# Kernel tuning notes

Measured on AMD Instinct MI355X. Metric: run time of the kernel, lower is better.

Reference implementation:

```python
import jax, jax.numpy as jnp
import numpy as np

N = 100000      # nodes
E = 500000      # edges
NODE_IN = 60
EDGE_IN = 8
H = 256         # hidden
L = 8           # GINEConv layers
G = 64          # graphs in batch
BN_EPS = 1e-5


def setup_inputs() -> dict:
    key = jax.random.key(0)
    ks = jax.random.split(key, 40)
    s = 0.05
    f32 = jnp.float32
    inp = {
        "x": jax.random.normal(ks[0], (N, NODE_IN), f32),
        "edge_index": jax.random.randint(ks[1], (2, E), 0, N),
        "edge_attr": jax.random.normal(ks[2], (E, EDGE_IN), f32),
        "batch": jnp.sort(jax.random.randint(ks[3], (N,), 0, G)),
        # x_proj: Linear(node_in->H) + BatchNorm1d (eval-mode running stats)
        "xproj_W": jax.random.normal(ks[4], (NODE_IN, H), f32) * s,
        "xproj_b": jnp.zeros((H,), f32),
        "xp_gamma": jnp.ones((H,), f32),
        "xp_beta": jnp.zeros((H,), f32),
        "xp_mean": jax.random.normal(ks[5], (H,), f32) * 0.01,
        "xp_var": jax.random.uniform(ks[6], (H,), f32, 0.5, 1.5),
        # stacked GINEConv params (L layers)
        "edge_W": jax.random.normal(ks[7], (L, EDGE_IN, H), f32) * s,
        "edge_b": jnp.zeros((L, H), f32),
        "mlp_W1": jax.random.normal(ks[8], (L, H, H), f32) * s,
        "mlp_b1": jnp.zeros((L, H), f32),
        "mlp_W2": jax.random.normal(ks[9], (L, H, H), f32) * s,
        "mlp_b2": jnp.zeros((L, H), f32),
        "eps": jnp.zeros((L,), f32),  # GINE eps (default 0, not trained)
        # per-layer BatchNorm (eval-mode)
        "bn_gamma": jnp.ones((L, H), f32),
        "bn_beta": jnp.zeros((L, H), f32),
        "bn_mean": jax.random.normal(ks[10], (L, H), f32) * 0.01,
        "bn_var": jax.random.uniform(ks[11], (L, H), f32, 0.5, 1.5),
        # head: Linear(H->H/2) ReLU Dropout Linear(H/2->1)
        "head_W1": jax.random.normal(ks[12], (H, H // 2), f32) * s,
        "head_b1": jnp.zeros((H // 2,), f32),
        "head_W2": jax.random.normal(ks[13], (H // 2, 1), f32) * s,
        "head_b2": jnp.zeros((1,), f32),
    }
    return inp


def _bn(x, gamma, beta, mean, var):
    # eval-mode BatchNorm1d with running stats
    return (x - mean) * (gamma * jax.lax.rsqrt(var + BN_EPS)) + beta


def reference(x, edge_index, edge_attr, batch,
              xproj_W, xproj_b, xp_gamma, xp_beta, xp_mean, xp_var,
              edge_W, edge_b, mlp_W1, mlp_b1, mlp_W2, mlp_b2, eps,
              bn_gamma, bn_beta, bn_mean, bn_var,
              head_W1, head_b1, head_W2, head_b2):
    src, dst = edge_index[0], edge_index[1]  # source -> target aggregation
    # x_proj: Linear + BN + ReLU
    h = jax.nn.relu(_bn(x @ xproj_W + xproj_b, xp_gamma, xp_beta, xp_mean, xp_var))
    for l in range(L):
        # GINEConv: msg = ReLU(x_j + lin(edge_attr)); sum-aggregate at target
        e = edge_attr @ edge_W[l] + edge_b[l]                 # [E,H]
        m = jax.nn.relu(h[src] + e)                           # [E,H] gather + add
        agg = jax.ops.segment_sum(m, dst, num_segments=N)     # [N,H] scatter-add
        z = (1.0 + eps[l]) * h + agg
        z = jax.nn.relu(z @ mlp_W1[l] + mlp_b1[l]) @ mlp_W2[l] + mlp_b2[l]
        # BN + ReLU (dropout is identity in eval)
        h = jax.nn.relu(_bn(z, bn_gamma[l], bn_beta[l], bn_mean[l], bn_var[l]))
    # global_mean_pool over batch ids
    gsum = jax.ops.segment_sum(h, batch, num_segments=G)      # [G,H]
    cnt = jax.ops.segment_sum(jnp.ones((N, 1), h.dtype), batch, num_segments=G)
    g = gsum / jnp.maximum(cnt, 1.0)
    # head MLP -> scalar per graph
    hid = jax.nn.relu(g @ head_W1 + head_b1)
    out = (hid @ head_W2 + head_b2)[:, 0]                     # [G]
    return out
```

## Files before the change

### kernel.cpp

```cpp
#include <hip/hip_runtime.h>

#define N_NODES 100000
#define N_EDGES 500000
#define NODE_IN 60
#define EDGE_IN 8
#define HID 256
#define NLAYERS 8
#define NGRAPH 64
#define BN_EPS 1e-5f
#define SY_PITCH 520

typedef __attribute__((ext_vector_type(4))) float f32x4;
typedef __attribute__((ext_vector_type(4))) short short4v;
typedef __attribute__((ext_vector_type(8))) short short8v;
typedef __attribute__((ext_vector_type(4))) unsigned short u16x4;
typedef unsigned short u16;

__device__ __forceinline__ u16 f2bf(float f) {
    unsigned int u = __builtin_bit_cast(unsigned int, f);
    u += 0x7fffu + ((u >> 16) & 1u);
    return (u16)(u >> 16);
}
__device__ __forceinline__ float bf2f(u16 u) {
    unsigned int x = ((unsigned int)u) << 16;
    return __builtin_bit_cast(float, x);
}
__device__ __forceinline__ float lo_f(unsigned int d) {
    return __builtin_bit_cast(float, d << 16);
}
__device__ __forceinline__ float hi_f(unsigned int d) {
    return __builtin_bit_cast(float, d & 0xffff0000u);
}

__device__ __forceinline__ void g2lds16(const void* g, void* l) {
    __builtin_amdgcn_global_load_lds(
        (const __attribute__((address_space(1))) void*)g,
        (__attribute__((address_space(3))) void*)l, 16, 0, 0);
}

template<int KT, bool WITH_BN>
__global__ __launch_bounds__(256, 2)
void mfma_gemm(const u16* A, const u16* Bt,
               const float* __restrict__ bias,
               const float* __restrict__ gamma, const float* __restrict__ beta,
               const float* __restrict__ mean,  const float* __restrict__ var,
               u16* Cout, int M)
{
    __shared__ u16 smem[24576];
    u16* sA = smem;
    u16* sB = smem + 8192;

    const int tid  = threadIdx.x;
    const int lane = tid & 63;
    const int wv   = tid >> 6;
    const int lrow = lane & 15;
    const int g    = lane >> 4;
    const int m0   = blockIdx.x * 128;
    const int ldab = KT * 128;
    const int lsub = lane >> 3;
    const int gsw  = ((lane & 7) * 16) ^ (lsub << 4);

    f32x4 acc[8][4] = {};

    for (int kt = 0; kt < KT; ++kt) {
        #pragma unroll
        for (int i = 0; i < 4; ++i) {
            const int row = i * 32 + wv * 8 + lsub;
            g2lds16((const char*)A + (size_t)(m0 + row) * ldab + kt * 128 + gsw,
                    (char*)sA + i * 4096 + wv * 1024);
        }
        #pragma unroll
        for (int i = 0; i < 8; ++i) {
            const int row = i * 32 + wv * 8 + lsub;
            g2lds16((const char*)Bt + (size_t)row * ldab + kt * 128 + gsw,
                    (char*)sB + i * 4096 + wv * 1024);
        }
        __syncthreads();

        #pragma unroll
        for (int ks = 0; ks < 2; ++ks) {
            const int off1 = ks * 64 + 8 * g;
            const int off2 = off1 + 32;
            short8v bfrag[4];
            #pragma unroll
            for (int nb = 0; nb < 4; ++nb) {
                const int col = wv * 64 + nb * 16 + lrow;
                const int sw  = (col & 7) << 4;
                short4v lo = *(const short4v*)((const char*)sB + col * 128 + (off1 ^ sw));
                short4v hi = *(const short4v*)((const char*)sB + col * 128 + (off2 ^ sw));
                short8v b;
                b[0] = lo[0]; b[1] = lo[1]; b[2] = lo[2]; b[3] = lo[3];
                b[4] = hi[0]; b[5] = hi[1]; b[6] = hi[2]; b[7] = hi[3];
                bfrag[nb] = b;
            }
            #pragma unroll
            for (int mb = 0; mb < 8; ++mb) {
                const int row = mb * 16 + lrow;
                const int sw  = (row & 7) << 4;
                short4v lo = *(const short4v*)((const char*)sA + row * 128 + (off1 ^ sw));
                short4v hi = *(const short4v*)((const char*)sA + row * 128 + (off2 ^ sw));
                short8v a;
                a[0] = lo[0]; a[1] = lo[1]; a[2] = lo[2]; a[3] = lo[3];
                a[4] = hi[0]; a[5] = hi[1]; a[6] = hi[2]; a[7] = hi[3];
                #pragma unroll
                for (int nb = 0; nb < 4; ++nb)
                    acc[mb][nb] = __builtin_amdgcn_mfma_f32_16x16x32_bf16(a, bfrag[nb], acc[mb][nb], 0, 0, 0);
            }
        }
        __syncthreads();
    }

    #pragma unroll
    for (int mb = 0; mb < 8; ++mb) {
        #pragma unroll
        for (int r = 0; r < 4; ++r) {
            const int row = m0 + mb * 16 + g * 4 + r;
            if (row >= M) continue;
            #pragma unroll
            for (int nb = 0; nb < 4; ++nb) {
                const int col = wv * 64 + nb * 16 + lrow;
                float v = acc[mb][nb][r] + bias[col];
                if constexpr (WITH_BN)
                    v = (v - mean[col]) * (gamma[col] * rsqrtf(var[col] + BN_EPS)) + beta[col];
                v = fmaxf(v, 0.f);
                Cout[(size_t)row * HID + col] = f2bf(v);
            }
        }
    }
}

__global__ __launch_bounds__(256, 2)
void fused_mlp(const u16* __restrict__ Z, const u16* __restrict__ W1t,
               const u16* __restrict__ W2t,
               const float* __restrict__ b1,
               const float* __restrict__ scale2, const float* __restrict__ shift2,
               u16* __restrict__ Hout, int M)
{
    __shared__ u16 smem[37120];
    u16* sA = smem;
    u16* sB = sA + 4096;
    u16* sY = sB + 16384;

    const int tid  = threadIdx.x;
    const int lane = tid & 63;
    const int wv   = tid >> 6;
    const int lrow = lane & 15;
    const int g    = lane >> 4;
    const int m0   = blockIdx.x * 64;
    const int lsub = lane >> 3;
    const int gsw  = ((lane & 7) * 16) ^ (lsub << 4);

    f32x4 acc[4][4] = {};

    for (int kt = 0; kt < 4; ++kt) {
        #pragma unroll
        for (int i = 0; i < 2; ++i) {
            const int row = i * 32 + wv * 8 + lsub;
            g2lds16((const char*)Z + (size_t)(m0 + row) * 512 + kt * 128 + gsw,
                    (char*)sA + i * 4096 + wv * 1024);
        }
        #pragma unroll
        for (int i = 0; i < 8; ++i) {
            const int row = i * 32 + wv * 8 + lsub;
            g2lds16((const char*)W1t + (size_t)row * 512 + kt * 128 + gsw,
                    (char*)sB + i * 4096 + wv * 1024);
        }
        __syncthreads();

        #pragma unroll
        for (int ks = 0; ks < 2; ++ks) {
            const int off1 = ks * 64 + 8 * g;
            const int off2 = off1 + 32;
            short8v bfrag[4];
            #pragma unroll
            for (int nb = 0; nb < 4; ++nb) {
                const int col = wv * 64 + nb * 16 + lrow;
                const int sw  = (col & 7) << 4;
                short4v lo = *(const short4v*)((const char*)sB + col * 128 + (off1 ^ sw));
                short4v hi = *(const short4v*)((const char*)sB + col * 128 + (off2 ^ sw));
                short8v b;
                b[0] = lo[0]; b[1] = lo[1]; b[2] = lo[2]; b[3] = lo[3];
                b[4] = hi[0]; b[5] = hi[1]; b[6] = hi[2]; b[7] = hi[3];
                bfrag[nb] = b;
            }
            #pragma unroll
            for (int mb = 0; mb < 4; ++mb) {
                const int row = mb * 16 + lrow;
                const int sw  = (row & 7) << 4;
                short4v lo = *(const short4v*)((const char*)sA + row * 128 + (off1 ^ sw));
                short4v hi = *(const short4v*)((const char*)sA + row * 128 + (off2 ^ sw));
                short8v a;
                a[0] = lo[0]; a[1] = lo[1]; a[2] = lo[2]; a[3] = lo[3];
                a[4] = hi[0]; a[5] = hi[1]; a[6] = hi[2]; a[7] = hi[3];
                #pragma unroll
                for (int nb = 0; nb < 4; ++nb)
                    acc[mb][nb] = __builtin_amdgcn_mfma_f32_16x16x32_bf16(a, bfrag[nb], acc[mb][nb], 0, 0, 0);
            }
        }
        __syncthreads();
    }

    float b1v[4];
    #pragma unroll
    for (int nb = 0; nb < 4; ++nb) b1v[nb] = b1[wv * 64 + nb * 16 + lrow];
    #pragma unroll
    for (int mb = 0; mb < 4; ++mb) {
        #pragma unroll
        for (int r = 0; r < 4; ++r) {
            const int row = mb * 16 + g * 4 + r;
            #pragma unroll
            for (int nb = 0; nb < 4; ++nb) {
                const int col = wv * 64 + nb * 16 + lrow;
                const float v = fmaxf(acc[mb][nb][r] + b1v[nb], 0.f);
                *(u16*)((char*)sY + row * SY_PITCH + col * 2) = f2bf(v);
            }
        }
    }
    __syncthreads();

    f32x4 acc2[4][4] = {};
    for (int kt2 = 0; kt2 < 4; ++kt2) {
        #pragma unroll
        for (int i = 0; i < 8; ++i) {
            const int row = i * 32 + wv * 8 + lsub;
            g2lds16((const char*)W2t + (size_t)row * 512 + kt2 * 128 + gsw,
                    (char*)sB + i * 4096 + wv * 1024);
        }
        __syncthreads();

        #pragma unroll
        for (int ks = 0; ks < 2; ++ks) {
            const int off1 = ks * 64 + 8 * g;
            const int off2 = off1 + 32;
            const int yo1  = kt2 * 128 + off1;
            const int yo2  = yo1 + 32;
            short8v bfrag[4];
            #pragma unroll
            for (int nb = 0; nb < 4; ++nb) {
                const int col = wv * 64 + nb * 16 + lrow;
                const int sw  = (col & 7) << 4;
                short4v lo = *(const short4v*)((const char*)sB + col * 128 + (off1 ^ sw));
                short4v hi = *(const short4v*)((const char*)sB + col * 128 + (off2 ^ sw));
                short8v b;
                b[0] = lo[0]; b[1] = lo[1]; b[2] = lo[2]; b[3] = lo[3];
                b[4] = hi[0]; b[5] = hi[1]; b[6] = hi[2]; b[7] = hi[3];
                bfrag[nb] = b;
            }
            #pragma unroll
            for (int mb = 0; mb < 4; ++mb) {
                const int row = mb * 16 + lrow;
                short4v lo = *(const short4v*)((const char*)sY + row * SY_PITCH + yo1);
                short4v hi = *(const short4v*)((const char*)sY + row * SY_PITCH + yo2);
                short8v a;
                a[0] = lo[0]; a[1] = lo[1]; a[2] = lo[2]; a[3] = lo[3];
                a[4] = hi[0]; a[5] = hi[1]; a[6] = hi[2]; a[7] = hi[3];
                #pragma unroll
                for (int nb = 0; nb < 4; ++nb)
                    acc2[mb][nb] = __builtin_amdgcn_mfma_f32_16x16x32_bf16(a, bfrag[nb], acc2[mb][nb], 0, 0, 0);
            }
        }
        __syncthreads();
    }

    float scl[4], shf[4];
    #pragma unroll
    for (int nb = 0; nb < 4; ++nb) {
        const int col = wv * 64 + nb * 16 + lrow;
        scl[nb] = scale2[col];
        shf[nb] = shift2[col];
    }
    #pragma unroll
    for (int mb = 0; mb < 4; ++mb) {
        #pragma unroll
        for (int r = 0; r < 4; ++r) {
            const int row = m0 + mb * 16 + g * 4 + r;
            if (row >= M) continue;
            #pragma unroll
            for (int nb = 0; nb < 4; ++nb) {
                const int col = wv * 64 + nb * 16 + lrow;
                const float v = fmaxf(acc2[mb][nb][r] * scl[nb] + shf[nb], 0.f);
                Hout[(size_t)row * HID + col] = f2bf(v);
            }
        }
    }
}

__global__ __launch_bounds__(256)
void convw_kernel(const float* __restrict__ W, u16* __restrict__ Wt)
{
    size_t i = (size_t)blockIdx.x * 256 + threadIdx.x;
    const int mat = (int)(i >> 16);
    const int idx = (int)(i & 65535);
    const int n = idx >> 8, k = idx & 255;
    Wt[i] = f2bf(W[(size_t)mat * 65536 + (size_t)k * 256 + n]);
}

__global__ __launch_bounds__(256)
void convwx_kernel(const float* __restrict__ W, u16* __restrict__ Wt)
{
    int i = blockIdx.x * 256 + threadIdx.x;
    const int n = i >> 6, k = i & 63;
    Wt[i] = (k < NODE_IN) ? f2bf(W[(size_t)k * HID + n]) : (u16)0;
}

__global__ __launch_bounds__(256)
void convx_kernel(const float* __restrict__ x, u16* __restrict__ xbf)
{
    size_t i = (size_t)blockIdx.x * 256 + threadIdx.x;
    if (i >= (size_t)N_NODES * 64) return;
    const int n = (int)(i >> 6), k = (int)(i & 63);
    xbf[i] = (k < NODE_IN) ? f2bf(x[(size_t)n * NODE_IN + k]) : (u16)0;
}

__global__ __launch_bounds__(256)
void bnfold_kernel(const float* __restrict__ b2, const float* __restrict__ gamma,
                   const float* __restrict__ beta, const float* __restrict__ mean,
                   const float* __restrict__ var,
                   float* __restrict__ scale, float* __restrict__ shift)
{
    int i = blockIdx.x * 256 + threadIdx.x;
    if (i >= NLAYERS * HID) return;
    const float s = gamma[i] * rsqrtf(var[i] + BN_EPS);
    scale[i] = s;
    shift[i] = (b2[i] - mean[i]) * s + beta[i];
}

__global__ __launch_bounds__(256)
void deg_count_kernel(const int* __restrict__ dst, int* __restrict__ deg, int E)
{
    int e = blockIdx.x * 256 + threadIdx.x;
    if (e < E) atomicAdd(&deg[dst[e]], 1);
}

__global__ __launch_bounds__(256)
void scan1_kernel(const int* __restrict__ deg, int* __restrict__ rowptr,
                  int* __restrict__ bsum, int n)
{
    __shared__ int s[256];
    const int tid = threadIdx.x;
    const int i = blockIdx.x * 256 + tid;
    const int v = (i < n) ? deg[i] : 0;
    s[tid] = v;
    __syncthreads();
    #pragma unroll
    for (int d = 1; d < 256; d <<= 1) {
        int t = (tid >= d) ? s[tid - d] : 0;
        __syncthreads();
        s[tid] += t;
        __syncthreads();
    }
    if (i < n) rowptr[i] = s[tid] - v;
    if (tid == 255) bsum[blockIdx.x] = s[255];
}

__global__ void scan2_kernel(int* bsum, int nb, int* rowptr, int n)
{
    if (threadIdx.x == 0 && blockIdx.x == 0) {
        int run = 0;
        for (int j = 0; j < nb; ++j) { int t = bsum[j]; bsum[j] = run; run += t; }
        rowptr[n] = run;
    }
}

__global__ __launch_bounds__(256)
void scan3_kernel(int* __restrict__ rowptr, const int* __restrict__ bsum, int n)
{
    int i = blockIdx.x * 256 + threadIdx.x;
    if (i < n) rowptr[i] += bsum[i >> 8];
}

__global__ __launch_bounds__(256)
void scatter_kernel(const int* __restrict__ src, const int* __restrict__ dst,
                    const float* __restrict__ ea,
                    const int* __restrict__ rowptr, int* __restrict__ fill,
                    int* __restrict__ esrc, u16* __restrict__ eap, int E)
{
    int e = blockIdx.x * 256 + threadIdx.x;
    if (e >= E) return;
    const int d = dst[e];
    const int pos = rowptr[d] + atomicAdd(&fill[d], 1);
    esrc[pos] = src[e];
    const float4 a0 = *(const float4*)&ea[(size_t)e * EDGE_IN];
    const float4 a1 = *(const float4*)&ea[(size_t)e * EDGE_IN + 4];
    u16x4 p0, p1;
    p0[0] = f2bf(a0.x); p0[1] = f2bf(a0.y); p0[2] = f2bf(a0.z); p0[3] = f2bf(a0.w);
    p1[0] = f2bf(a1.x); p1[1] = f2bf(a1.y); p1[2] = f2bf(a1.z); p1[3] = f2bf(a1.w);
    *(u16x4*)&eap[(size_t)pos * EDGE_IN]     = p0;
    *(u16x4*)&eap[(size_t)pos * EDGE_IN + 4] = p1;
}

__global__ __launch_bounds__(256, 8)
void agg_kernel(const u16* __restrict__ h, const u16* __restrict__ eap,
                const int* __restrict__ rowptr, const int* __restrict__ esrc,
                const float* __restrict__ W, const float* __restrict__ b,
                const float* __restrict__ eps, int l, u16* __restrict__ z)
{
    const int lane  = threadIdx.x & 63;
    const int wv    = threadIdx.x >> 6;
    const int c0    = lane * 4;
    const int lofsB = lane * 8;

    f32x4 Wr[EDGE_IN];
    #pragma unroll
    for (int k = 0; k < EDGE_IN; ++k) Wr[k] = *(const f32x4*)&W[k * HID + c0];
    const f32x4 br = *(const f32x4*)&b[c0];
    const float e1 = 1.0f + eps[l];

    for (int n = blockIdx.x * 4 + wv; n < N_NODES; n += gridDim.x * 4) {
        const int beg = __builtin_amdgcn_readfirstlane(rowptr[n]);
        const int end = __builtin_amdgcn_readfirstlane(rowptr[n + 1]);
        const int end1 = end - 1;

        const u16x4 hv = *(const u16x4*)&h[(size_t)n * HID + c0];
        float a0 = e1 * bf2f(hv[0]), a1 = e1 * bf2f(hv[1]);
        float a2 = e1 * bf2f(hv[2]), a3 = e1 * bf2f(hv[3]);

        for (int i0 = beg; i0 < end; i0 += 4) {
            int idx0 = i0;
            int idx1 = (i0 + 1 < end) ? i0 + 1 : end1;
            int idx2 = (i0 + 2 < end) ? i0 + 2 : end1;
            int idx3 = (i0 + 3 < end) ? i0 + 3 : end1;

            const int sb0 = __builtin_amdgcn_readfirstlane(esrc[idx0]) << 9;
            const int sb1 = __builtin_amdgcn_readfirstlane(esrc[idx1]) << 9;
            const int sb2 = __builtin_amdgcn_readfirstlane(esrc[idx2]) << 9;
            const int sb3 = __builtin_amdgcn_readfirstlane(esrc[idx3]) << 9;

            u16x4 hs0 = *(const u16x4*)((const char*)h + (unsigned)(sb0 + lofsB));
            u16x4 hs1 = *(const u16x4*)((const char*)h + (unsigned)(sb1 + lofsB));
            u16x4 hs2 = *(const u16x4*)((const char*)h + (unsigned)(sb2 + lofsB));
            u16x4 hs3 = *(const u16x4*)((const char*)h + (unsigned)(sb3 + lofsB));

            uint4 t0 = *(const uint4*)&eap[(size_t)idx0 * EDGE_IN];
            uint4 t1 = *(const uint4*)&eap[(size_t)idx1 * EDGE_IN];
            uint4 t2 = *(const uint4*)&eap[(size_t)idx2 * EDGE_IN];
            uint4 t3 = *(const uint4*)&eap[(size_t)idx3 * EDGE_IN];

            #pragma unroll
            for (int j = 0; j < 4; ++j) {
                if (i0 + j < end) {
                    const uint4 tt = (j == 0) ? t0 : (j == 1) ? t1 : (j == 2) ? t2 : t3;
                    const u16x4 hh = (j == 0) ? hs0 : (j == 1) ? hs1 : (j == 2) ? hs2 : hs3;
                    const unsigned dx = __builtin_amdgcn_readfirstlane((int)tt.x);
                    const unsigned dy = __builtin_amdgcn_readfirstlane((int)tt.y);
                    const unsigned dz = __builtin_amdgcn_readfirstlane((int)tt.z);
                    const unsigned dw = __builtin_amdgcn_readfirstlane((int)tt.w);
                    f32x4 ev = br;
                    ev += lo_f(dx) * Wr[0];
                    ev += hi_f(dx) * Wr[1];
                    ev += lo_f(dy) * Wr[2];
                    ev += hi_f(dy) * Wr[3];
                    ev += lo_f(dz) * Wr[4];
                    ev += hi_f(dz) * Wr[5];
                    ev += lo_f(dw) * Wr[6];
                    ev += hi_f(dw) * Wr[7];
                    a0 += fmaxf(bf2f(hh[0]) + ev[0], 0.f);
                    a1 += fmaxf(bf2f(hh[1]) + ev[1], 0.f);
                    a2 += fmaxf(bf2f(hh[2]) + ev[2], 0.f);
                    a3 += fmaxf(bf2f(hh[3]) + ev[3], 0.f);
                }
            }
        }
        u16x4 o;
        o[0] = f2bf(a0); o[1] = f2bf(a1); o[2] = f2bf(a2); o[3] = f2bf(a3);
        *(u16x4*)&z[(size_t)n * HID + c0] = o;
    }
}

__global__ __launch_bounds__(256)
void pool_kernel(const u16* __restrict__ h, const int* __restrict__ batch,
                 float* __restrict__ gsum, int* __restrict__ cnt, int n)
{
    const int lane = threadIdx.x & 63;
    const int wv   = threadIdx.x >> 6;
    const int c0   = lane * 4;
    const int n0   = blockIdx.x * 64;

    f32x4 acc = {0.f, 0.f, 0.f, 0.f};
    int gcur = -1;
    int c = 0;

    for (int i = wv; i < 64; i += 4) {
        const int node = n0 + i;
        if (node >= n) break;
        const int g = __builtin_amdgcn_readfirstlane(batch[node]);
        if (g != gcur) {
            if (gcur >= 0) {
                atomicAdd(&gsum[gcur * HID + c0 + 0], acc[0]);
                atomicAdd(&gsum[gcur * HID + c0 + 1], acc[1]);
                atomicAdd(&gsum[gcur * HID + c0 + 2], acc[2]);
                atomicAdd(&gsum[gcur * HID + c0 + 3], acc[3]);
                if (lane == 0) atomicAdd(&cnt[gcur], c);
            }
            acc = (f32x4){0.f, 0.f, 0.f, 0.f};
            c = 0;
            gcur = g;
        }
        const u16x4 hv = *(const u16x4*)&h[(size_t)node * HID + c0];
        acc[0] += bf2f(hv[0]);
        acc[1] += bf2f(hv[1]);
        acc[2] += bf2f(hv[2]);
        acc[3] += bf2f(hv[3]);
        c++;
    }
    if (gcur >= 0) {
        atomicAdd(&gsum[gcur * HID + c0 + 0], acc[0]);
        atomicAdd(&gsum[gcur * HID + c0 + 1], acc[1]);
        atomicAdd(&gsum[gcur * HID + c0 + 2], acc[2]);
        atomicAdd(&gsum[gcur * HID + c0 + 3], acc[3]);
        if (lane == 0) atomicAdd(&cnt[gcur], c);
    }
}

__global__ __launch_bounds__(128)
void head_kernel(const float* __restrict__ gsum, const int* __restrict__ cnt,
                 const float* __restrict__ W1, const float* __restrict__ b1,
                 const float* __restrict__ W2, const float* __restrict__ b2,
                 float* __restrict__ out)
{
    const int gi = blockIdx.x;
    const int j = threadIdx.x;
    __shared__ float gs[HID];
    __shared__ float red[128];

    const float c = fmaxf((float)cnt[gi], 1.0f);
    gs[j]       = gsum[gi * HID + j] / c;
    gs[j + 128] = gsum[gi * HID + 128 + j] / c;
    __syncthreads();

    float acc = b1[j];
    #pragma unroll 8
    for (int k = 0; k < HID; ++k) acc += gs[k] * W1[k * 128 + j];
    acc = fmaxf(acc, 0.f);
    red[j] = acc * W2[j];
    __syncthreads();
    for (int s = 64; s > 0; s >>= 1) {
        if (j < s) red[j] += red[j + s];
        __syncthreads();
    }
    if (j == 0) out[gi] = red[0] + b2[0];
}

extern "C" void kernel_launch(void* const* d_in, const int* in_sizes, int n_in,
                              void* d_out, int out_size, void* d_ws, size_t ws_size,
                              hipStream_t stream)
{
    const float* x         = (const float*)d_in[0];
    const int*   ei        = (const int*)d_in[1];
    const float* edge_attr = (const float*)d_in[2];
    const int*   batch     = (const int*)d_in[3];
    const float* xproj_W   = (const float*)d_in[4];
    const float* xproj_b   = (const float*)d_in[5];
    const float* xp_gamma  = (const float*)d_in[6];
    const float* xp_beta   = (const float*)d_in[7];
    const float* xp_mean   = (const float*)d_in[8];
    const float* xp_var    = (const float*)d_in[9];
    const float* edge_W    = (const float*)d_in[10];
    const float* edge_b    = (const float*)d_in[11];
    const float* mlp_W1    = (const float*)d_in[12];
    const float* mlp_b1    = (const float*)d_in[13];
    const float* mlp_W2    = (const float*)d_in[14];
    const float* mlp_b2    = (const float*)d_in[15];
    const float* eps       = (const float*)d_in[16];
    const float* bn_gamma  = (const float*)d_in[17];
    const float* bn_beta   = (const float*)d_in[18];
    const float* bn_mean   = (const float*)d_in[19];
    const float* bn_var    = (const float*)d_in[20];
    const float* head_W1   = (const float*)d_in[21];
    const float* head_b1   = (const float*)d_in[22];
    const float* head_W2   = (const float*)d_in[23];
    const float* head_b2   = (const float*)d_in[24];
    float* out = (float*)d_out;

    const int* srcI = ei;
    const int* dstI = ei + N_EDGES;

    char* w = (char*)d_ws;
    u16*   h      = (u16*)w;                 w += (size_t)N_NODES * HID * 2;
    u16*   zy     = (u16*)w;                 w += (size_t)N_NODES * HID * 2;
    u16*   xbf    = (u16*)w;                 w += (size_t)N_NODES * 64 * 2;
    u16*   Wt1    = (u16*)w;                 w += (size_t)NLAYERS * 65536 * 2;
    u16*   Wt2    = (u16*)w;                 w += (size_t)NLAYERS * 65536 * 2;
    u16*   Wxt    = (u16*)w;                 w += 16384 * 2;
    float* scale2 = (float*)w;               w += NLAYERS * HID * 4;
    float* shift2 = (float*)w;               w += NLAYERS * HID * 4;
    int*   rowptr = (int*)w;                 w += 100032 * 4;
    int*   deg    = (int*)w;                 w += 100032 * 4;
    int*   fill   = (int*)w;                 w += 100032 * 4;
    int*   bsum   = (int*)w;                 w += 512 * 4;
    int*   esrc   = (int*)w;                 w += (size_t)N_EDGES * 4;
    u16*   eap    = (u16*)w;                 w += (size_t)N_EDGES * EDGE_IN * 2;
    float* gsum   = (float*)w;               w += NGRAPH * HID * 4;
    int*   cnt    = (int*)w;                 w += NGRAPH * 4;

    convw_kernel<<<2048, 256, 0, stream>>>(mlp_W1, Wt1);
    convw_kernel<<<2048, 256, 0, stream>>>(mlp_W2, Wt2);
    convwx_kernel<<<64, 256, 0, stream>>>(xproj_W, Wxt);
    convx_kernel<<<25000, 256, 0, stream>>>(x, xbf);
    bnfold_kernel<<<8, 256, 0, stream>>>(mlp_b2, bn_gamma, bn_beta, bn_mean, bn_var,
                                         scale2, shift2);

    hipMemsetAsync(deg, 0, 2 * 100032 * sizeof(int), stream);
    deg_count_kernel<<<(N_EDGES + 255) / 256, 256, 0, stream>>>(dstI, deg, N_EDGES);
    scan1_kernel<<<391, 256, 0, stream>>>(deg, rowptr, bsum, N_NODES);
    scan2_kernel<<<1, 64, 0, stream>>>(bsum, 391, rowptr, N_NODES);
    scan3_kernel<<<391, 256, 0, stream>>>(rowptr, bsum, N_NODES);
    scatter_kernel<<<(N_EDGES + 255) / 256, 256, 0, stream>>>(
        srcI, dstI, edge_attr, rowptr, fill, esrc, eap, N_EDGES);

    mfma_gemm<1, true><<<(N_NODES + 127) / 128, 256, 0, stream>>>(
        xbf, Wxt, xproj_b, xp_gamma, xp_beta, xp_mean, xp_var, h, N_NODES);

    const int fgrid = (N_NODES + 63) / 64;
    for (int l = 0; l < NLAYERS; ++l) {
        agg_kernel<<<2048, 256, 0, stream>>>(
            h, eap, rowptr, esrc,
            edge_W + (size_t)l * EDGE_IN * HID, edge_b + (size_t)l * HID,
            eps, l, zy);
        fused_mlp<<<fgrid, 256, 0, stream>>>(
            zy, Wt1 + (size_t)l * 65536, Wt2 + (size_t)l * 65536,
            mlp_b1 + (size_t)l * HID, scale2 + (size_t)l * HID, shift2 + (size_t)l * HID,
            h, N_NODES);
    }

    hipMemsetAsync(gsum, 0, (NGRAPH * HID + NGRAPH) * sizeof(float), stream);
    pool_kernel<<<(N_NODES + 63) / 64, 256, 0, stream>>>(h, batch, gsum, cnt, N_NODES);
    head_kernel<<<NGRAPH, 128, 0, stream>>>(gsum, cnt, head_W1, head_b1, head_W2, head_b2, out);
}
```

Baseline: 1.126 ms.

## Prepack MLP weights in MFMA fragment order and read them directly from global

Weights are repacked at setup into per-lane MFMA B-fragment order, so the fused MLP kernel loads B fragments straight from global memory (cached in L2/L1) instead of staging the full 256x256 weight tiles through LDS every k-step. The whole 64-row Z tile is loaded once up front, and shared memory is cut to about 33KB with sZ and sY aliased, which removes per-k-step barriers. Occupancy is raised to 3 blocks per SM. The trade-off is that every block now does redundant global/L1 reads of the weights and depends on cache hit rates, and the higher occupancy target may cause register pressure.

Measured after the change: 1.064 ms, median of 3. 1.06x faster.

```diff
diff --git a/kernel.cpp b/kernel.cpp
--- a/kernel.cpp
+++ b/kernel.cpp
@@ -129,17 +129,16 @@
     }
 }
 
-__global__ __launch_bounds__(256, 2)
-void fused_mlp(const u16* __restrict__ Z, const u16* __restrict__ W1t,
-               const u16* __restrict__ W2t,
+__global__ __launch_bounds__(256, 3)
+void fused_mlp(const u16* __restrict__ Z, const u16* __restrict__ W1p,
+               const u16* __restrict__ W2p,
                const float* __restrict__ b1,
                const float* __restrict__ scale2, const float* __restrict__ shift2,
                u16* __restrict__ Hout, int M)
 {
-    __shared__ u16 smem[37120];
-    u16* sA = smem;
-    u16* sB = sA + 4096;
-    u16* sY = sB + 16384;
+    __shared__ u16 smem[16640];
+    u16* sZ = smem;
+    u16* sY = smem;
 
     const int tid  = threadIdx.x;
     const int lane = tid & 63;
@@ -150,23 +149,20 @@
     const int lsub = lane >> 3;
     const int gsw  = ((lane & 7) * 16) ^ (lsub << 4);
 
-    f32x4 acc[4][4] = {};
-
+    #pragma unroll
     for (int kt = 0; kt < 4; ++kt) {
         #pragma unroll
         for (int i = 0; i < 2; ++i) {
             const int row = i * 32 + wv * 8 + lsub;
             g2lds16((const char*)Z + (size_t)(m0 + row) * 512 + kt * 128 + gsw,
-                    (char*)sA + i * 4096 + wv * 1024);
-        }
-        #pragma unroll
-        for (int i = 0; i < 8; ++i) {
-            const int row = i * 32 + wv * 8 + lsub;
-            g2lds16((const char*)W1t + (size_t)row * 512 + kt * 128 + gsw,
-                    (char*)sB + i * 4096 + wv * 1024);
-        }
-        __syncthreads();
-
+                    (char*)sZ + kt * 8192 + i * 4096 + wv * 1024);
+        }
+    }
+    __syncthreads();
+
+    f32x4 acc[4][4] = {};
+    #pragma unroll
+    for (int kt = 0; kt < 4; ++kt) {
         #pragma unroll
         for (int ks = 0; ks < 2; ++ks) {
             const int off1 = ks * 64 + 8 * g;
@@ -174,21 +170,20 @@
             short8v bfrag[4];
             #pragma unroll
             for (int nb = 0; nb < 4; ++nb) {
-                const int col = wv * 64 + nb * 16 + lrow;
-                const int sw  = (col & 7) << 4;
-                short4v lo = *(const short4v*)((const char*)sB + col * 128 + (off1 ^ sw));
-                short4v hi = *(const short4v*)((const char*)sB + col * 128 + (off2 ^ sw));
+                const int cb = wv * 4 + nb;
+                u16x4 lo = *(const u16x4*)&W1p[((((kt * 2 + ks) * 2 + 0) * 16 + cb) << 8) + lane * 4];
+                u16x4 hi = *(const u16x4*)&W1p[((((kt * 2 + ks) * 2 + 1) * 16 + cb) << 8) + lane * 4];
                 short8v b;
-                b[0] = lo[0]; b[1] = lo[1]; b[2] = lo[2]; b[3] = lo[3];
-                b[4] = hi[0]; b[5] = hi[1]; b[6] = hi[2]; b[7] = hi[3];
+                b[0] = (short)lo[0]; b[1] = (short)lo[1]; b[2] = (short)lo[2]; b[3] = (short)lo[3];
+                b[4] = (short)hi[0]; b[5] = (short)hi[1]; b[6] = (short)hi[2]; b[7] = (short)hi[3];
                 bfrag[nb] = b;
             }
             #pragma unroll
             for (int mb = 0; mb < 4; ++mb) {
                 const int row = mb * 16 + lrow;
                 const int sw  = (row & 7) << 4;
-                short4v lo = *(const short4v*)((const char*)sA + row * 128 + (off1 ^ sw));
-                short4v hi = *(const short4v*)((const char*)sA + row * 128 + (off2 ^ sw));
+                short4v lo = *(const short4v*)((const char*)sZ + kt * 8192 + row * 128 + (off1 ^ sw));
+                short4v hi = *(const short4v*)((const char*)sZ + kt * 8192 + row * 128 + (off2 ^ sw));
                 short8v a;
                 a[0] = lo[0]; a[1] = lo[1]; a[2] = lo[2]; a[3] = lo[3];
                 a[4] = hi[0]; a[5] = hi[1]; a[6] = hi[2]; a[7] = hi[3];
@@ -197,8 +192,8 @@
                     acc[mb][nb] = __builtin_amdgcn_mfma_f32_16x16x32_bf16(a, bfrag[nb], acc[mb][nb], 0, 0, 0);
             }
         }
-        __syncthreads();
-    }
+    }
+    __syncthreads();
 
     float b1v[4];
     #pragma unroll
@@ -219,31 +214,22 @@
     __syncthreads();
 
     f32x4 acc2[4][4] = {};
+    #pragma unroll
     for (int kt2 = 0; kt2 < 4; ++kt2) {
-        #pragma unroll
-        for (int i = 0; i < 8; ++i) {
-            const int row = i * 32 + wv * 8 + lsub;
-            g2lds16((const char*)W2t + (size_t)row * 512 + kt2 * 128 + gsw,
-                    (char*)sB + i * 4096 + wv * 1024);
-        }
-        __syncthreads();
-
         #pragma unroll
         for (int ks = 0; ks < 2; ++ks) {
             const int off1 = ks * 64 + 8 * g;
-            const int off2 = off1 + 32;
             const int yo1  = kt2 * 128 + off1;
             const int yo2  = yo1 + 32;
             short8v bfrag[4];
             #pragma unroll
             for (int nb = 0; nb < 4; ++nb) {
-                const int col = wv * 64 + nb * 16 + lrow;
-                const int sw  = (col & 7) << 4;
-                short4v lo = *(const short4v*)((const char*)sB + col * 128 + (off1 ^ sw));
-                short4v hi = *(const short4v*)((const char*)sB + col * 128 + (off2 ^ sw));
+                const int cb = wv * 4 + nb;
+                u16x4 lo = *(const u16x4*)&W2p[((((kt2 * 2 + ks) * 2 + 0) * 16 + cb) << 8) + lane * 4];
+                u16x4 hi = *(const u16x4*)&W2p[((((kt2 * 2 + ks) * 2 + 1) * 16 + cb) << 8) + lane * 4];
                 short8v b;
-                b[0] = lo[0]; b[1] = lo[1]; b[2] = lo[2]; b[3] = lo[3];
-                b[4] = hi[0]; b[5] = hi[1]; b[6] = hi[2]; b[7] = hi[3];
+                b[0] = (short)lo[0]; b[1] = (short)lo[1]; b[2] = (short)lo[2]; b[3] = (short)lo[3];
+                b[4] = (short)hi[0]; b[5] = (short)hi[1]; b[6] = (short)hi[2]; b[7] = (short)hi[3];
                 bfrag[nb] = b;
             }
             #pragma unroll
@@ -259,7 +245,6 @@
                     acc2[mb][nb] = __builtin_amdgcn_mfma_f32_16x16x32_bf16(a, bfrag[nb], acc2[mb][nb], 0, 0, 0);
             }
         }
-        __syncthreads();
     }
 
     float scl[4], shf[4];
@@ -286,13 +271,20 @@
 }
 
 __global__ __launch_bounds__(256)
-void convw_kernel(const float* __restrict__ W, u16* __restrict__ Wt)
+void convw_kernel(const float* __restrict__ W, u16* __restrict__ Wp)
 {
     size_t i = (size_t)blockIdx.x * 256 + threadIdx.x;
-    const int mat = (int)(i >> 16);
-    const int idx = (int)(i & 65535);
-    const int n = idx >> 8, k = idx & 255;
-    Wt[i] = f2bf(W[(size_t)mat * 65536 + (size_t)k * 256 + n]);
+    const int mat  = (int)(i >> 16);
+    const int r    = (int)(i & 65535);
+    const int j    = r & 3;
+    const int lane = (r >> 2) & 63;
+    const int cb   = (r >> 8) & 15;
+    const int half = (r >> 12) & 1;
+    const int ks   = (r >> 13) & 1;
+    const int kt   = (r >> 14) & 3;
+    const int col = cb * 16 + (lane & 15);
+    const int k   = kt * 64 + ks * 32 + 4 * (lane >> 4) + 16 * half + j;
+    Wp[i] = f2bf(W[(size_t)mat * 65536 + (size_t)k * 256 + col]);
 }
 
 __global__ __launch_bounds__(256)
@@ -579,8 +571,8 @@
     u16*   h      = (u16*)w;                 w += (size_t)N_NODES * HID * 2;
     u16*   zy     = (u16*)w;                 w += (size_t)N_NODES * HID * 2;
     u16*   xbf    = (u16*)w;                 w += (size_t)N_NODES * 64 * 2;
-    u16*   Wt1    = (u16*)w;                 w += (size_t)NLAYERS * 65536 * 2;
-    u16*   Wt2    = (u16*)w;                 w += (size_t)NLAYERS * 65536 * 2;
+    u16*   Wp1    = (u16*)w;                 w += (size_t)NLAYERS * 65536 * 2;
+    u16*   Wp2    = (u16*)w;                 w += (size_t)NLAYERS * 65536 * 2;
     u16*   Wxt    = (u16*)w;                 w += 16384 * 2;
     float* scale2 = (float*)w;               w += NLAYERS * HID * 4;
     float* shift2 = (float*)w;               w += NLAYERS * HID * 4;
@@ -593,8 +585,8 @@
     float* gsum   = (float*)w;               w += NGRAPH * HID * 4;
     int*   cnt    = (int*)w;                 w += NGRAPH * 4;
 
-    convw_kernel<<<2048, 256, 0, stream>>>(mlp_W1, Wt1);
-    convw_kernel<<<2048, 256, 0, stream>>>(mlp_W2, Wt2);
+    convw_kernel<<<2048, 256, 0, stream>>>(mlp_W1, Wp1);
+    convw_kernel<<<2048, 256, 0, stream>>>(mlp_W2, Wp2);
     convwx_kernel<<<64, 256, 0, stream>>>(xproj_W, Wxt);
     convx_kernel<<<25000, 256, 0, stream>>>(x, xbf);
     bnfold_kernel<<<8, 256, 0, stream>>>(mlp_b2, bn_gamma, bn_beta, bn_mean, bn_var,
@@ -618,7 +610,7 @@
             edge_W + (size_t)l * EDGE_IN * HID, edge_b + (size_t)l * HID,
             eps, l, zy);
         fused_mlp<<<fgrid, 256, 0, stream>>>(
-            zy, Wt1 + (size_t)l * 65536, Wt2 + (size_t)l * 65536,
+            zy, Wp1 + (size_t)l * 65536, Wp2 + (size_t)l * 65536,
             mlp_b1 + (size_t)l * HID, scale2 + (size_t)l * HID, shift2 + (size_t)l * HID,
             h, N_NODES);
     }
```
